# Optimization experiments

Hardware: AMD Instinct MI355X
Metric: run time of the kernel (lower is better)

## Reference

```python
import jax, jax.numpy as jnp
import numpy as np

FILL = -100  # SentimentClasses.FILLUP_POLARITY_VALUE, also CrossEntropyLoss ignore_index
B, T, S, C = 512, 8, 8192, 3


def setup_inputs() -> dict:
    key = jax.random.key(0)
    k1, k2, k3 = jax.random.split(key, 3)
    predictions = jax.random.normal(k1, (B, C, S), dtype=jnp.float32)
    true_classes = jax.random.randint(k2, (B, T), 0, 3, dtype=jnp.int64)
    raw = jax.random.randint(k3, (B, T, S), 0, 2, dtype=jnp.int64)
    # keep at most one target per (batch, seq) position so the original's
    # conflict check would never fire (mask rows are disjoint)
    cum = jnp.cumsum(raw, axis=1)
    true_target_mask = ((raw == 1) & (cum == 1)).astype(jnp.int64)
    return {"predictions": predictions, "true_classes": true_classes,
            "true_target_mask": true_target_mask}


def reference(predictions, true_classes, true_target_mask):
    # Vectorized replacement of the nested scatter loop:
    # position (b,s) gets class of the (unique) target whose mask is 1, else FILL.
    valid_t = (true_classes != FILL)[:, :, None] & (true_target_mask == 1)  # [B,T,S]
    true_sequence = jnp.max(
        jnp.where(valid_t, true_classes[:, :, None], FILL), axis=1)  # [B,S]

    # CrossEntropyLoss(ignore_index=FILL) over class axis (axis=1)
    logp = jax.nn.log_softmax(predictions, axis=1)  # [B,C,S]
    valid = true_sequence != FILL  # [B,S]
    tgt_safe = jnp.where(valid, true_sequence, 0)
    nll = -jnp.take_along_axis(logp, tgt_safe[:, None, :], axis=1)[:, 0, :]  # [B,S]
    n_valid = jnp.maximum(jnp.sum(valid), 1).astype(nll.dtype)
    return jnp.sum(jnp.where(valid, nll, 0.0)) / n_valid
```

## Files before the change

kernel.cpp:

```cpp
#include <hip/hip_runtime.h>

namespace {

constexpr int FILL = -100;
constexpr int B = 512, T = 8, S = 8192, C = 3;
constexpr int VEC = 4;
constexpr int THREADS = 256;
constexpr int SB = S / VEC;
constexpr int NGROUPS = B * SB;
constexpr int BLOCKS = 2048;

__global__ __launch_bounds__(THREADS) void seq_loss_partial(
    const float4* __restrict__ predv,
    const int*    __restrict__ cls,
    const int4*   __restrict__ maskv,
    float* __restrict__ part_sum,
    int*   __restrict__ part_cnt)
{
    float lsum = 0.0f;
    int   lcnt = 0;

    for (int gid = blockIdx.x * THREADS + threadIdx.x; gid < NGROUPS;
         gid += BLOCKS * THREADS) {
        const int b  = gid >> 11;
        const int s4 = gid & (SB - 1);

        int4 m[T];
        #pragma unroll
        for (int t = 0; t < T; ++t)
            m[t] = maskv[(b * T + t) * SB + s4];

        const float4 p0 = predv[(b * C + 0) * SB + s4];
        const float4 p1 = predv[(b * C + 1) * SB + s4];
        const float4 p2 = predv[(b * C + 2) * SB + s4];

        int c[T];
        #pragma unroll
        for (int t = 0; t < T; ++t)
            c[t] = cls[b * T + t];

        int tgt0 = FILL, tgt1 = FILL, tgt2 = FILL, tgt3 = FILL;
        #pragma unroll
        for (int t = 0; t < T; ++t) {
            const bool cv = (c[t] != FILL);
            if (cv & (m[t].x == 1)) tgt0 = max(tgt0, c[t]);
            if (cv & (m[t].y == 1)) tgt1 = max(tgt1, c[t]);
            if (cv & (m[t].z == 1)) tgt2 = max(tgt2, c[t]);
            if (cv & (m[t].w == 1)) tgt3 = max(tgt3, c[t]);
        }

        auto acc = [&](int tgt, float x0, float x1, float x2) {
            if (tgt != FILL) {
                const float lse = __logf(__expf(x0) + __expf(x1) + __expf(x2));
                const float xt  = (tgt == 0) ? x0 : ((tgt == 1) ? x1 : x2);
                lsum += lse - xt;
                ++lcnt;
            }
        };
        acc(tgt0, p0.x, p1.x, p2.x);
        acc(tgt1, p0.y, p1.y, p2.y);
        acc(tgt2, p0.z, p1.z, p2.z);
        acc(tgt3, p0.w, p1.w, p2.w);
    }

    #pragma unroll
    for (int off = 32; off > 0; off >>= 1) {
        lsum += __shfl_down(lsum, off);
        lcnt += __shfl_down(lcnt, off);
    }
    __shared__ float sm_s[THREADS / 64];
    __shared__ int   sm_c[THREADS / 64];
    const int lane = threadIdx.x & 63, wv = threadIdx.x >> 6;
    if (lane == 0) { sm_s[wv] = lsum; sm_c[wv] = lcnt; }
    __syncthreads();
    if (threadIdx.x == 0) {
        float s = 0.0f; int cc = 0;
        #pragma unroll
        for (int i = 0; i < THREADS / 64; ++i) { s += sm_s[i]; cc += sm_c[i]; }
        part_sum[blockIdx.x] = s;
        part_cnt[blockIdx.x] = cc;
    }
}

__global__ __launch_bounds__(256) void seq_loss_final(
    const float* __restrict__ part_sum,
    const int*   __restrict__ part_cnt,
    float*       __restrict__ out)
{
    double s = 0.0, c = 0.0;
    for (int i = threadIdx.x; i < BLOCKS; i += 256) {
        s += (double)part_sum[i];
        c += (double)part_cnt[i];
    }
    #pragma unroll
    for (int off = 32; off > 0; off >>= 1) {
        s += __shfl_down(s, off);
        c += __shfl_down(c, off);
    }
    __shared__ double ds[4], dc[4];
    const int lane = threadIdx.x & 63, wv = threadIdx.x >> 6;
    if (lane == 0) { ds[wv] = s; dc[wv] = c; }
    __syncthreads();
    if (threadIdx.x == 0) {
        double st = ds[0] + ds[1] + ds[2] + ds[3];
        double ct = dc[0] + dc[1] + dc[2] + dc[3];
        if (ct < 1.0) ct = 1.0;
        out[0] = (float)(st / ct);
    }
}

}

extern "C" void kernel_launch(void* const* d_in, const int* in_sizes, int n_in,
                              void* d_out, int out_size, void* d_ws, size_t ws_size,
                              hipStream_t stream) {
    const float4* predv = (const float4*)d_in[0];
    const int*    cls   = (const int*)d_in[1];
    const int4*   maskv = (const int4*)d_in[2];

    float* part_sum = (float*)d_ws;
    int*   part_cnt = (int*)((char*)d_ws + BLOCKS * sizeof(float));
    float* out      = (float*)d_out;

    seq_loss_partial<<<BLOCKS, THREADS, 0, stream>>>(predv, cls, maskv,
                                                     part_sum, part_cnt);
    seq_loss_final<<<1, 256, 0, stream>>>(part_sum, part_cnt, out);
}
```

Measured before the change: 222.0 us.

## Issue both batch halves' loads up front with nontemporal hints and multiply-sum target decode

Replaces the grid-stride loop with a fixed mapping where each thread handles two batch rows, issuing all mask and prediction loads before any compute to raise memory-level parallelism. Loads use nontemporal hints to avoid polluting caches with streamed data. Target decoding becomes a multiply-accumulate of mask by (class+1), which assumes mask entries are 0/1 and at most one target per position, unlike the reference's max semantics. Register pressure rises from holding sixteen mask vectors at once.

```diff
diff --git a/kernel.cpp b/kernel.cpp
--- a/kernel.cpp
+++ b/kernel.cpp
@@ -4,64 +4,76 @@
 
 constexpr int FILL = -100;
 constexpr int B = 512, T = 8, S = 8192, C = 3;
-constexpr int VEC = 4;
 constexpr int THREADS = 256;
-constexpr int SB = S / VEC;
-constexpr int NGROUPS = B * SB;
+constexpr int SB = S / 4;
 constexpr int BLOCKS = 2048;
 
+typedef int   iv4 __attribute__((ext_vector_type(4)));
+typedef float fv4 __attribute__((ext_vector_type(4)));
+
 __global__ __launch_bounds__(THREADS) void seq_loss_partial(
-    const float4* __restrict__ predv,
-    const int*    __restrict__ cls,
-    const int4*   __restrict__ maskv,
+    const fv4* __restrict__ predv,
+    const int* __restrict__ cls,
+    const iv4* __restrict__ maskv,
     float* __restrict__ part_sum,
     int*   __restrict__ part_cnt)
 {
+    const int b0 = blockIdx.x >> 3;
+    const int b1 = b0 + 256;
+    const int s4 = ((blockIdx.x & 7) << 8) + threadIdx.x;
+
+    iv4 m0[T], m1[T];
+    #pragma unroll
+    for (int t = 0; t < T; ++t)
+        m0[t] = __builtin_nontemporal_load(&maskv[(b0 * T + t) * SB + s4]);
+    #pragma unroll
+    for (int t = 0; t < T; ++t)
+        m1[t] = __builtin_nontemporal_load(&maskv[(b1 * T + t) * SB + s4]);
+
+    const fv4 a0 = __builtin_nontemporal_load(&predv[(b0 * C + 0) * SB + s4]);
+    const fv4 a1 = __builtin_nontemporal_load(&predv[(b0 * C + 1) * SB + s4]);
+    const fv4 a2 = __builtin_nontemporal_load(&predv[(b0 * C + 2) * SB + s4]);
+    const fv4 d0 = __builtin_nontemporal_load(&predv[(b1 * C + 0) * SB + s4]);
+    const fv4 d1 = __builtin_nontemporal_load(&predv[(b1 * C + 1) * SB + s4]);
+    const fv4 d2 = __builtin_nontemporal_load(&predv[(b1 * C + 2) * SB + s4]);
+
+    int ce0[T], ce1[T];
+    #pragma unroll
+    for (int t = 0; t < T; ++t) {
+        const int c0 = cls[b0 * T + t];
+        const int c1 = cls[b1 * T + t];
+        ce0[t] = (c0 != FILL) ? (c0 + 1) : 0;
+        ce1[t] = (c1 != FILL) ? (c1 + 1) : 0;
+    }
+
     float lsum = 0.0f;
     int   lcnt = 0;
 
-    for (int gid = blockIdx.x * THREADS + threadIdx.x; gid < NGROUPS;
-         gid += BLOCKS * THREADS) {
-        const int b  = gid >> 11;
-        const int s4 = gid & (SB - 1);
-
-        int4 m[T];
-        #pragma unroll
-        for (int t = 0; t < T; ++t)
-            m[t] = maskv[(b * T + t) * SB + s4];
-
-        const float4 p0 = predv[(b * C + 0) * SB + s4];
-        const float4 p1 = predv[(b * C + 1) * SB + s4];
-        const float4 p2 = predv[(b * C + 2) * SB + s4];
-
-        int c[T];
-        #pragma unroll
-        for (int t = 0; t < T; ++t)
-            c[t] = cls[b * T + t];
-
-        int tgt0 = FILL, tgt1 = FILL, tgt2 = FILL, tgt3 = FILL;
+    auto consume = [&](const iv4* m, const int* ce,
+                       const fv4& p0, const fv4& p1, const fv4& p2) {
+        int sx = 0, sy = 0, sz = 0, sw = 0;
         #pragma unroll
         for (int t = 0; t < T; ++t) {
-            const bool cv = (c[t] != FILL);
-            if (cv & (m[t].x == 1)) tgt0 = max(tgt0, c[t]);
-            if (cv & (m[t].y == 1)) tgt1 = max(tgt1, c[t]);
-            if (cv & (m[t].z == 1)) tgt2 = max(tgt2, c[t]);
-            if (cv & (m[t].w == 1)) tgt3 = max(tgt3, c[t]);
+            sx += m[t].x * ce[t];
+            sy += m[t].y * ce[t];
+            sz += m[t].z * ce[t];
+            sw += m[t].w * ce[t];
         }
-
-        auto acc = [&](int tgt, float x0, float x1, float x2) {
-            if (tgt != FILL) {
+        auto acc = [&](int sum, float x0, float x1, float x2) {
+            if (sum > 0) {
                 const float lse = __logf(__expf(x0) + __expf(x1) + __expf(x2));
-                const float xt  = (tgt == 0) ? x0 : ((tgt == 1) ? x1 : x2);
+                const float xt  = (sum == 1) ? x0 : ((sum == 2) ? x1 : x2);
                 lsum += lse - xt;
                 ++lcnt;
             }
         };
-        acc(tgt0, p0.x, p1.x, p2.x);
-        acc(tgt1, p0.y, p1.y, p2.y);
-        acc(tgt2, p0.z, p1.z, p2.z);
-        acc(tgt3, p0.w, p1.w, p2.w);
-    }
+        acc(sx, p0.x, p1.x, p2.x);
+        acc(sy, p0.y, p1.y, p2.y);
+        acc(sz, p0.z, p1.z, p2.z);
+        acc(sw, p0.w, p1.w, p2.w);
+    };
+    consume(m0, ce0, a0, a1, a2);
+    consume(m1, ce1, d0, d1, d2);
 
     #pragma unroll
     for (int off = 32; off > 0; off >>= 1) {
@@ -114,9 +126,9 @@
 extern "C" void kernel_launch(void* const* d_in, const int* in_sizes, int n_in,
                               void* d_out, int out_size, void* d_ws, size_t ws_size,
                               hipStream_t stream) {
-    const float4* predv = (const float4*)d_in[0];
-    const int*    cls   = (const int*)d_in[1];
-    const int4*   maskv = (const int4*)d_in[2];
+    const fv4* predv = (const fv4*)d_in[0];
+    const int* cls   = (const int*)d_in[1];
+    const iv4* maskv = (const iv4*)d_in[2];
 
     float* part_sum = (float*)d_ws;
     int*   part_cnt = (int*)((char*)d_ws + BLOCKS * sizeof(float));
```

After: 208.5 us. -6.1%, faster.
